# Optimization experiments

Measured on AMD Instinct MI355X. Metric: run time of the kernel, lower is better.

Reference implementation:

```python
import jax, jax.numpy as jnp
import numpy as np

B, N, D_IN, D_MEM = 32, 1024, 512, 512
LN_EPS = 1e-5


def setup_inputs() -> dict:
    key = jax.random.key(0)
    ks = jax.random.split(key, 6)
    adj = jax.random.uniform(ks[0], (B, N, N), dtype=jnp.float32)
    input_emb = jax.random.normal(ks[1], (B * N, D_IN), dtype=jnp.float32)
    seq_lens = jnp.full((B,), N, dtype=jnp.int64) if jax.config.jax_enable_x64 else jnp.full((B,), N, dtype=jnp.int32)
    scale = 1.0 / np.sqrt(D_IN)
    W0_w = jax.random.normal(ks[2], (D_MEM, D_IN), dtype=jnp.float32) * scale
    W0_b = jax.random.normal(ks[3], (D_MEM,), dtype=jnp.float32) * 0.01
    W1_w = jax.random.normal(ks[4], (D_MEM, D_MEM), dtype=jnp.float32) * scale
    W1_b = jax.random.normal(ks[5], (D_MEM,), dtype=jnp.float32) * 0.01
    ln_g = jnp.ones((D_MEM,), dtype=jnp.float32)
    ln_b = jnp.zeros((D_MEM,), dtype=jnp.float32)
    return {"adj": adj, "input_emb": input_emb, "seq_lens": seq_lens,
            "W0_w": W0_w, "W0_b": W0_b, "W1_w": W1_w, "W1_b": W1_b,
            "ln_g": ln_g, "ln_b": ln_b}


def _layer_norm(x, g, b):
    mu = jnp.mean(x, axis=-1, keepdims=True)
    var = jnp.mean(jnp.square(x - mu), axis=-1, keepdims=True)
    return (x - mu) * jax.lax.rsqrt(var + LN_EPS) * g + b


def reference(adj, input_emb, seq_lens, W0_w, W0_b, W1_w, W1_b, ln_g, ln_b):
    # All seq_lens == N, so pad_sequence(split(input_emb)) is a pure reshape.
    x = input_emb.reshape(B, N, D_IN)  # dropout probs are 0 -> identity
    denom = jnp.sum(adj, axis=2, keepdims=True) + 1.0           # [B,N,1]
    masks = ((jnp.sum(adj, axis=2) + jnp.sum(adj, axis=1)) == 0)[..., None]  # [B,N,1]
    for Ww, Wb in ((W0_w, W0_b), (W1_w, W1_b)):
        Ax = jnp.einsum('bnm,bmd->bnd', adj, x)                 # adj.bmm(x)
        # W(Ax) + W(x) == (Ax + x) @ W^T + 2b
        AxW = (Ax + x) @ Ww.T + 2.0 * Wb
        x = jax.nn.relu(AxW / denom)                            # gcn_drop p=0
    out = _layer_norm(x, ln_g, ln_b)                            # norm_flag=True
    return out, masks
```

## Files before the change

### kernel.cpp

```cpp
#include <hip/hip_runtime.h>
#include <stdint.h>

typedef __bf16 bf16_t;
typedef __bf16 bf16x8 __attribute__((ext_vector_type(8)));
typedef float  f32x4  __attribute__((ext_vector_type(4)));

#define GLD_LDS(gp, lp) __builtin_amdgcn_global_load_lds( \
    (const __attribute__((address_space(1))) void*)(gp),  \
    (__attribute__((address_space(3))) void*)(lp), 16, 0, 0)

__global__ void probe_kernel(const unsigned int* __restrict__ w, int* __restrict__ flag)
{
    const int lane = threadIdx.x;
    bool ok = true;
#pragma unroll
    for (int i = 0; i < 4; ++i) {
        unsigned x = w[lane * 4 + i];
        unsigned lo = x & 0xffffu, hi = x >> 16;
        ok = ok && (lo <= 0x3F80u) && (hi <= 0x3F80u);
    }
    unsigned long long m = __ballot(ok);
    if (lane == 0) *flag = (m == ~0ULL) ? 1 : 0;
}

#define STAGE_HALF(dstE, gp) do { \
    GLD_LDS((gp) + (size_t)r0 * K + cS,        lds + (dstE) + t * 8); \
    GLD_LDS((gp) + (size_t)(r0 + 64) * K + cS, lds + (dstE) + 4096 + t * 8); } while (0)

#define STG_A(d, h, k0) STAGE_HALF((d)*16384 + (h)*8192, Ag + (size_t)(h)*128*K + (k0))
#define STG_B(d, h, k0) STAGE_HALF(32768 + (d)*16384 + (h)*8192, Bg + (size_t)(h)*128*K + (k0))

#define LDA(af, d, mq) do { _Pragma("unroll") for (int i_ = 0; i_ < 4; ++i_) { \
    const bf16_t* p_ = lds + (d)*16384 + aBase + (((mq)*64) + (i_ << 4) + lrow) * 64; \
    af[i_][0] = *(const bf16x8*)(p_ + so0); \
    af[i_][1] = *(const bf16x8*)(p_ + so1); } } while (0)

#define LDB(bfv, d, nq) do { _Pragma("unroll") for (int j_ = 0; j_ < 2; ++j_) { \
    const bf16_t* p_ = lds + bBase + (d)*16384 + (((nq)*32) + (j_ << 4) + lrow) * 64; \
    bfv[j_][0] = *(const bf16x8*)(p_ + so0); \
    bfv[j_][1] = *(const bf16x8*)(p_ + so1); } } while (0)

#define MFMA_Q(af, bfv, mq, nq) do { _Pragma("unroll") for (int i_ = 0; i_ < 4; ++i_) \
    _Pragma("unroll") for (int j_ = 0; j_ < 2; ++j_) { \
    acc[(mq)*4+i_][(nq)*2+j_] = __builtin_amdgcn_mfma_f32_16x16x32_bf16(af[i_][0], bfv[j_][0], acc[(mq)*4+i_][(nq)*2+j_], 0, 0, 0); \
    acc[(mq)*4+i_][(nq)*2+j_] = __builtin_amdgcn_mfma_f32_16x16x32_bf16(af[i_][1], bfv[j_][1], acc[(mq)*4+i_][(nq)*2+j_], 0, 0, 0); } } while (0)

#define PHASE_SYNC() do { __builtin_amdgcn_s_barrier(); \
    asm volatile("s_waitcnt lgkmcnt(0)" ::: "memory"); \
    __builtin_amdgcn_sched_barrier(0); \
    __builtin_amdgcn_s_setprio(1); } while (0)

#define PHASE_END() do { __builtin_amdgcn_s_setprio(0); \
    __builtin_amdgcn_s_barrier(); } while (0)

#define PHASE_END_VM() do { __builtin_amdgcn_s_setprio(0); \
    asm volatile("s_waitcnt vmcnt(4)" ::: "memory"); \
    __builtin_amdgcn_s_barrier(); } while (0)

__device__ __forceinline__ void gemm256_mainloop(const bf16_t* __restrict__ Ag,
                                                 const bf16_t* __restrict__ Bg,
                                                 const int K, bf16_t* lds,
                                                 f32x4 acc[8][4])
{
    const int t    = threadIdx.x;
    const int wave = t >> 6;
    const int lane = t & 63;
    const int wr   = wave >> 2;
    const int wc   = wave & 3;
    const int lrow = lane & 15;
    const int quad = lane >> 4;
    const int g    = lrow & 7;

    const int r0 = t >> 3;
    const int cS = ((t & 7) ^ ((t >> 3) & 7)) << 3;

    const int aBase = wr * 8192;
    const int bBase = 32768 + ((wc >> 1) * 8192) + ((wc & 1) * 4096);
    const int so0 = (quad ^ g) << 3;
    const int so1 = ((4 | quad) ^ g) << 3;

#pragma unroll
    for (int i = 0; i < 8; ++i)
#pragma unroll
        for (int j = 0; j < 4; ++j)
#pragma unroll
            for (int r = 0; r < 4; ++r) acc[i][j][r] = 0.0f;

    STG_A(0, 0, 0); STG_A(0, 1, 0);
    STG_B(0, 0, 0); STG_B(0, 1, 0);
    STG_B(1, 0, 64); STG_B(1, 1, 64);
    asm volatile("s_waitcnt vmcnt(4)" ::: "memory");
    __builtin_amdgcn_s_barrier();

    const int NT  = K >> 6;
    const int NIT = NT >> 1;

    bf16x8 af0[4][2], af1[4][2], ba[2][2], bb[2][2];

    for (int it = 0; it < NIT; ++it) {
        const int kA1 = (2 * it + 1) << 6;
        const int k2  = ((2 * it + 2) < NT ? (2 * it + 2) : 0) << 6;
        const int k3  = ((2 * it + 3) < NT ? (2 * it + 3) : 0) << 6;

        LDA(af0, 0, 0); LDB(ba, 0, 0); STG_A(1, 0, kA1);
        PHASE_SYNC(); MFMA_Q(af0, ba, 0, 0); PHASE_END();

        LDB(bb, 0, 1); STG_A(1, 1, kA1);
        PHASE_SYNC(); MFMA_Q(af0, bb, 0, 1); PHASE_END();

        LDA(af1, 0, 1); STG_B(0, 0, k2);
        PHASE_SYNC(); MFMA_Q(af1, ba, 1, 0); PHASE_END();

        STG_B(0, 1, k2);
        PHASE_SYNC(); MFMA_Q(af1, bb, 1, 1); PHASE_END_VM();

        LDA(af0, 1, 0); LDB(ba, 1, 0); STG_A(0, 0, k2);
        PHASE_SYNC(); MFMA_Q(af0, ba, 0, 0); PHASE_END();

        LDB(bb, 1, 1); STG_A(0, 1, k2);
        PHASE_SYNC(); MFMA_Q(af0, bb, 0, 1); PHASE_END();

        LDA(af1, 1, 1); STG_B(1, 0, k3);
        PHASE_SYNC(); MFMA_Q(af1, ba, 1, 0); PHASE_END();

        STG_B(1, 1, k3);
        PHASE_SYNC(); MFMA_Q(af1, bb, 1, 1); PHASE_END_VM();
    }
    asm volatile("s_waitcnt vmcnt(0)" ::: "memory");
}

__global__ __launch_bounds__(512, 2) void bmm_kernel(const void* __restrict__ adj_in,
                                                     const bf16_t* __restrict__ adj_ws,
                                                     const bf16_t* __restrict__ xT,
                                                     const void* __restrict__ xadd,
                                                     int xadd_bf16,
                                                     const int* __restrict__ flag,
                                                     bf16_t* __restrict__ zout)
{
    extern __shared__ __align__(16) bf16_t lds[];
    const int is_bf = *flag;
    const bf16_t* adj = is_bf ? (const bf16_t*)adj_in : adj_ws;
    const int id   = blockIdx.x;
    const int xcd  = id & 7;
    const int s    = id >> 3;
    const int b    = (xcd << 2) | (s >> 3);
    const int tl   = s & 7;
    const int mt   = tl >> 1;
    const int nt2  = tl & 1;
    const bf16_t* Ag = adj + (size_t)b * 1048576 + (size_t)mt * 262144;
    const bf16_t* Bg = xT  + (size_t)b * 524288  + (size_t)nt2 * 262144;
    f32x4 acc[8][4];
    gemm256_mainloop(Ag, Bg, 1024, lds, acc);

    const int lane = threadIdx.x & 63;
    const int wave = threadIdx.x >> 6;
    const int wr = wave >> 2, wc = wave & 3;
    const int lrow = lane & 15, quad = lane >> 4;
    const int xf32 = (!xadd_bf16) && (!is_bf);
    const size_t rowbase = (size_t)b * 1024 + mt * 256 + wr * 128;
    const int colbase = nt2 * 256 + wc * 64;
#pragma unroll
    for (int i = 0; i < 8; ++i)
#pragma unroll
        for (int j = 0; j < 4; ++j)
#pragma unroll
            for (int r = 0; r < 4; ++r) {
                size_t row = rowbase + (i << 4) + (quad << 2) + r;
                int col = colbase + (j << 4) + lrow;
                size_t idx = row * 512 + col;
                float xa = xf32 ? ((const float*)xadd)[idx]
                                : (float)((const bf16_t*)xadd)[idx];
                zout[idx] = (bf16_t)(acc[i][j][r] + xa);
            }
}

__global__ __launch_bounds__(512, 2) void wgemm_kernel(const bf16_t* __restrict__ z,
                                                       const bf16_t* __restrict__ W,
                                                       const float* __restrict__ bias,
                                                       const float* __restrict__ rowsum,
                                                       bf16_t* __restrict__ out)
{
    extern __shared__ __align__(16) bf16_t lds[];
    const int id  = blockIdx.x;
    const int xcd = id & 7;
    const int s   = id >> 3;
    const int mt  = (xcd << 4) | (s >> 1);
    const int nt2 = s & 1;
    const bf16_t* Ag = z + (size_t)mt * 131072;
    const bf16_t* Bg = W + (size_t)nt2 * 131072;
    f32x4 acc[8][4];
    gemm256_mainloop(Ag, Bg, 512, lds, acc);

    const int lane = threadIdx.x & 63;
    const int wave = threadIdx.x >> 6;
    const int wr = wave >> 2, wc = wave & 3;
    const int lrow = lane & 15, quad = lane >> 4;
    const int m0 = mt * 256 + wr * 128;
    const int n0 = nt2 * 256 + wc * 64;
    float bi[4];
#pragma unroll
    for (int j = 0; j < 4; ++j) bi[j] = 2.0f * bias[n0 + (j << 4) + lrow];
#pragma unroll
    for (int i = 0; i < 8; ++i)
#pragma unroll
        for (int r = 0; r < 4; ++r) {
            int row = m0 + (i << 4) + (quad << 2) + r;
            float inv_dn = 1.0f / (rowsum[row] + 1.0f);
#pragma unroll
            for (int j = 0; j < 4; ++j) {
                int col = n0 + (j << 4) + lrow;
                float v = fmaxf((acc[i][j][r] + bi[j]) * inv_dn, 0.0f);
                out[(size_t)row * 512 + col] = (bf16_t)v;
            }
        }
}

__global__ __launch_bounds__(256) void transpose_kernel(const void* __restrict__ in,
                                                        bf16_t* __restrict__ out,
                                                        const int* __restrict__ flag,
                                                        int force_bf16)
{
    __shared__ float tile[64][65];
    const int f32 = (!force_bf16) && (*flag == 0);
    const int b  = blockIdx.z;
    const int n0 = blockIdx.x * 64;
    const int d0 = blockIdx.y * 64;
    const int t  = threadIdx.x;
    const size_t base = ((size_t)b * 1024 + n0) * 512 + d0;
#pragma unroll
    for (int pass = 0; pass < 2; ++pass) {
        int r = pass * 32 + (t >> 3);
        int c = (t & 7) << 3;
        size_t off = base + (size_t)r * 512 + c;
        if (f32) {
            const float4* p = (const float4*)((const float*)in + off);
            float4 a = p[0], q = p[1];
            tile[r][c+0]=a.x; tile[r][c+1]=a.y; tile[r][c+2]=a.z; tile[r][c+3]=a.w;
            tile[r][c+4]=q.x; tile[r][c+5]=q.y; tile[r][c+6]=q.z; tile[r][c+7]=q.w;
        } else {
            bf16x8 v = *(const bf16x8*)((const bf16_t*)in + off);
#pragma unroll
            for (int k = 0; k < 8; ++k) tile[r][c + k] = (float)v[k];
        }
    }
    __syncthreads();
    bf16_t* dst = out + ((size_t)b * 512 + d0) * 1024 + n0;
#pragma unroll
    for (int pass = 0; pass < 2; ++pass) {
        int d = pass * 32 + (t >> 3);
        int c = (t & 7) << 3;
        bf16x8 v;
#pragma unroll
        for (int k = 0; k < 8; ++k) v[k] = (bf16_t)tile[c + k][d];
        *(bf16x8*)(dst + (size_t)d * 1024 + c) = v;
    }
}

__global__ __launch_bounds__(256) void adjrow_kernel(const void* __restrict__ adj,
                                                     const int* __restrict__ flag,
                                                     bf16_t* __restrict__ adj_b,
                                                     float* __restrict__ rowsum)
{
    const int row  = blockIdx.x * 4 + (threadIdx.x >> 6);
    const int lane = threadIdx.x & 63;
    const int f32  = (*flag == 0);
    const size_t base = (size_t)row * 1024 + lane * 16;
    float v[16];
    if (f32) {
        const float4* p = (const float4*)((const float*)adj + base);
#pragma unroll
        for (int i = 0; i < 4; ++i) {
            float4 q = p[i];
            v[i*4+0]=q.x; v[i*4+1]=q.y; v[i*4+2]=q.z; v[i*4+3]=q.w;
        }
    } else {
        const bf16x8* p = (const bf16x8*)((const bf16_t*)adj + base);
        bf16x8 q0 = p[0], q1 = p[1];
#pragma unroll
        for (int k = 0; k < 8; ++k) { v[k] = (float)q0[k]; v[8+k] = (float)q1[k]; }
    }
    float s = 0.0f;
#pragma unroll
    for (int k = 0; k < 16; ++k) s += v[k];
    if (f32) {
        bf16x8 o0, o1;
#pragma unroll
        for (int k = 0; k < 8; ++k) { o0[k] = (bf16_t)v[k]; o1[k] = (bf16_t)v[8+k]; }
        *(bf16x8*)(adj_b + base)     = o0;
        *(bf16x8*)(adj_b + base + 8) = o1;
    }
#pragma unroll
    for (int off = 32; off > 0; off >>= 1) s += __shfl_down(s, off);
    if (lane == 0) rowsum[row] = s;
}

__global__ __launch_bounds__(256) void colsum_kernel(const void* __restrict__ adj_in,
                                                     const bf16_t* __restrict__ adj_ws,
                                                     const int* __restrict__ flag,
                                                     float* __restrict__ colsum)
{
    const bf16_t* a = (*flag) ? (const bf16_t*)adj_in : adj_ws;
    const int b = blockIdx.y;
    const int c = blockIdx.x * 256 + threadIdx.x;
    const int r0 = blockIdx.z * 256;
    const bf16_t* p = a + (size_t)b * 1048576 + (size_t)r0 * 1024 + c;
    float s = 0.0f;
#pragma unroll 8
    for (int r = 0; r < 256; ++r) s += (float)p[(size_t)r * 1024];
    atomicAdd(&colsum[b * 1024 + c], s);
}

__global__ __launch_bounds__(256) void mask_kernel(const float* __restrict__ rowsum,
                                                   const float* __restrict__ colsum,
                                                   void* __restrict__ out,
                                                   const int* __restrict__ flag)
{
    const int i = blockIdx.x * 256 + threadIdx.x;
    float m = (rowsum[i] + colsum[i] == 0.0f) ? 1.0f : 0.0f;
    if (*flag) ((bf16_t*)out)[16777216 + i] = (bf16_t)m;
    else       ((float*)out)[16777216 + i]  = m;
}

__global__ __launch_bounds__(256) void canon_small(const void* __restrict__ W0,
                                                   const void* __restrict__ W1,
                                                   const void* __restrict__ b0,
                                                   const void* __restrict__ b1,
                                                   const void* __restrict__ g,
                                                   const void* __restrict__ bt,
                                                   const int* __restrict__ flag,
                                                   bf16_t* __restrict__ W0ws,
                                                   bf16_t* __restrict__ W1ws,
                                                   float* __restrict__ par,
                                                   float* __restrict__ colsum)
{
    const int idx = blockIdx.x * 256 + threadIdx.x;
    const int f32 = (*flag == 0);
#define RD(p, i) (f32 ? ((const float*)(p))[i] : (float)((const bf16_t*)(p))[i])
    if      (idx < 262144) W0ws[idx]          = (bf16_t)RD(W0, idx);
    else if (idx < 524288) W1ws[idx - 262144] = (bf16_t)RD(W1, idx - 262144);
    else if (idx < 524800) par[idx - 524288]  = RD(b0, idx - 524288);
    else if (idx < 525312) par[idx - 524288]  = RD(b1, idx - 524800);
    else if (idx < 525824) par[idx - 524288]  = RD(g,  idx - 525312);
    else if (idx < 526336) par[idx - 524288]  = RD(bt, idx - 525824);
    else if (idx < 559104) colsum[idx - 526336] = 0.0f;
#undef RD
}

__global__ __launch_bounds__(256) void ln_kernel(const bf16_t* __restrict__ x,
                                                 const float* __restrict__ g,
                                                 const float* __restrict__ bb,
                                                 void* __restrict__ out,
                                                 const int* __restrict__ flag)
{
    const int row  = blockIdx.x * 4 + (threadIdx.x >> 6);
    const int lane = threadIdx.x & 63;
    bf16x8 xv = *(const bf16x8*)(x + (size_t)row * 512 + lane * 8);
    float vv[8], s = 0.0f, ss = 0.0f;
#pragma unroll
    for (int k = 0; k < 8; ++k) { vv[k] = (float)xv[k]; s += vv[k]; ss += vv[k] * vv[k]; }
#pragma unroll
    for (int off = 32; off > 0; off >>= 1) { s += __shfl_down(s, off); ss += __shfl_down(ss, off); }
    s = __shfl(s, 0); ss = __shfl(ss, 0);
    const float mu   = s * (1.0f / 512.0f);
    const float var  = ss * (1.0f / 512.0f) - mu * mu;
    const float rstd = rsqrtf(var + 1e-5f);
    float o[8];
#pragma unroll
    for (int k = 0; k < 8; ++k)
        o[k] = (vv[k] - mu) * rstd * g[lane * 8 + k] + bb[lane * 8 + k];
    const size_t obase = (size_t)row * 512 + lane * 8;
    if (*flag) {
        bf16x8 ob;
#pragma unroll
        for (int k = 0; k < 8; ++k) ob[k] = (bf16_t)o[k];
        *(bf16x8*)((bf16_t*)out + obase) = ob;
    } else {
        float4 o0 = {o[0], o[1], o[2], o[3]}, o1 = {o[4], o[5], o[6], o[7]};
        *(float4*)((float*)out + obase)     = o0;
        *(float4*)((float*)out + obase + 4) = o1;
    }
}

extern "C" void kernel_launch(void* const* d_in, const int* in_sizes, int n_in,
                              void* d_out, int out_size, void* d_ws, size_t ws_size,
                              hipStream_t stream)
{
    const void* adj  = d_in[0];
    const void* x0   = d_in[1];
    const void* W0w  = d_in[3];
    const void* W0b  = d_in[4];
    const void* W1w  = d_in[5];
    const void* W1b  = d_in[6];
    const void* lng  = d_in[7];
    const void* lnb  = d_in[8];

    char* ws = (char*)d_ws;
    bf16_t* adj_ws = (bf16_t*)ws;
    bf16_t* x2     = (bf16_t*)ws;
    bf16_t* z_buf  = (bf16_t*)(ws + 67108864);
    bf16_t* x1     = (bf16_t*)(ws + 100663296);
    bf16_t* W0ws   = (bf16_t*)(ws + 134217728);
    bf16_t* W1ws   = (bf16_t*)(ws + 134742016);
    float*  par    = (float*)(ws + 135266304);
    float*  rowsum = (float*)(ws + 135274496);
    float*  colsum = (float*)(ws + 135405568);
    int*    flag   = (int*)(ws + 135536640);

    bf16_t* xT = (bf16_t*)d_out;

    hipFuncSetAttribute((const void*)bmm_kernel,
                        hipFuncAttributeMaxDynamicSharedMemorySize, 131072);
    hipFuncSetAttribute((const void*)wgemm_kernel,
                        hipFuncAttributeMaxDynamicSharedMemorySize, 131072);

    probe_kernel<<<1, 64, 0, stream>>>((const unsigned int*)adj, flag);
    canon_small<<<2184, 256, 0, stream>>>(W0w, W1w, W0b, W1b, lng, lnb, flag,
                                          W0ws, W1ws, par, colsum);
    adjrow_kernel<<<8192, 256, 0, stream>>>(adj, flag, adj_ws, rowsum);
    colsum_kernel<<<dim3(4, 32, 4), 256, 0, stream>>>(adj, adj_ws, flag, colsum);
    mask_kernel<<<128, 256, 0, stream>>>(rowsum, colsum, d_out, flag);

    transpose_kernel<<<dim3(16, 8, 32), 256, 0, stream>>>(x0, xT, flag, 0);
    bmm_kernel<<<256, 512, 131072, stream>>>(adj, adj_ws, xT, x0, 0, flag, z_buf);
    wgemm_kernel<<<256, 512, 131072, stream>>>(z_buf, W0ws, par, rowsum, x1);

    transpose_kernel<<<dim3(16, 8, 32), 256, 0, stream>>>(x1, xT, flag, 1);
    bmm_kernel<<<256, 512, 131072, stream>>>(adj, adj_ws, xT, x1, 1, flag, z_buf);
    wgemm_kernel<<<256, 512, 131072, stream>>>(z_buf, W1ws, par + 512, rowsum, x2);

    ln_kernel<<<8192, 256, 0, stream>>>(x2, par + 1024, par + 1536, d_out, flag);
}
```

Measured before the change: 492.9 us.

## Fuse colsum into adjrow pass and emit transposed activations from wgemm epilogue

The row-sum and column-sum passes over adj become one kernel: each block walks 64 rows, keeps per-column partial sums in registers, and does four atomic adds per thread, so adj is read once instead of twice. The first-layer wgemm epilogue also writes the transposed bf16 activations directly, which removes the separate transpose kernel between layers. The risks are per-row shuffle reductions plus poorly coalesced 8-byte transposed stores from the GEMM epilogue.

```diff
diff --git a/kernel.cpp b/kernel.cpp
--- a/kernel.cpp
+++ b/kernel.cpp
@@ -2,6 +2,7 @@
 #include <stdint.h>
 
 typedef __bf16 bf16_t;
+typedef __bf16 bf16x4 __attribute__((ext_vector_type(4)));
 typedef __bf16 bf16x8 __attribute__((ext_vector_type(8)));
 typedef float  f32x4  __attribute__((ext_vector_type(4)));
 
@@ -178,7 +179,8 @@
                                                        const bf16_t* __restrict__ W,
                                                        const float* __restrict__ bias,
                                                        const float* __restrict__ rowsum,
-                                                       bf16_t* __restrict__ out)
+                                                       bf16_t* __restrict__ out,
+                                                       bf16_t* __restrict__ xTout)
 {
     extern __shared__ __align__(16) bf16_t lds[];
     const int id  = blockIdx.x;
@@ -197,22 +199,30 @@
     const int lrow = lane & 15, quad = lane >> 4;
     const int m0 = mt * 256 + wr * 128;
     const int n0 = nt2 * 256 + wc * 64;
+    bf16_t* xtb = xTout ? (xTout + (size_t)(mt >> 2) * 524288) : (bf16_t*)0;
     float bi[4];
 #pragma unroll
     for (int j = 0; j < 4; ++j) bi[j] = 2.0f * bias[n0 + (j << 4) + lrow];
 #pragma unroll
-    for (int i = 0; i < 8; ++i)
-#pragma unroll
-        for (int r = 0; r < 4; ++r) {
-            int row = m0 + (i << 4) + (quad << 2) + r;
-            float inv_dn = 1.0f / (rowsum[row] + 1.0f);
-#pragma unroll
-            for (int j = 0; j < 4; ++j) {
-                int col = n0 + (j << 4) + lrow;
-                float v = fmaxf((acc[i][j][r] + bi[j]) * inv_dn, 0.0f);
-                out[(size_t)row * 512 + col] = (bf16_t)v;
+    for (int i = 0; i < 8; ++i) {
+        const int rowb = m0 + (i << 4) + (quad << 2);
+        float invd[4];
+#pragma unroll
+        for (int r = 0; r < 4; ++r) invd[r] = 1.0f / (rowsum[rowb + r] + 1.0f);
+#pragma unroll
+        for (int j = 0; j < 4; ++j) {
+            const int col = n0 + (j << 4) + lrow;
+            bf16x4 tv;
+#pragma unroll
+            for (int r = 0; r < 4; ++r) {
+                float v = fmaxf((acc[i][j][r] + bi[j]) * invd[r], 0.0f);
+                bf16_t bv = (bf16_t)v;
+                out[(size_t)(rowb + r) * 512 + col] = bv;
+                tv[r] = bv;
             }
+            if (xtb) *(bf16x4*)(xtb + (size_t)col * 1024 + (rowb & 1023)) = tv;
         }
+    }
 }
 
 __global__ __launch_bounds__(256) void transpose_kernel(const void* __restrict__ in,
@@ -259,55 +269,44 @@
 __global__ __launch_bounds__(256) void adjrow_kernel(const void* __restrict__ adj,
                                                      const int* __restrict__ flag,
                                                      bf16_t* __restrict__ adj_b,
-                                                     float* __restrict__ rowsum)
-{
-    const int row  = blockIdx.x * 4 + (threadIdx.x >> 6);
+                                                     float* __restrict__ rowsum,
+                                                     float* __restrict__ colsum)
+{
+    __shared__ float rpart[64][4];
+    const int f32  = (*flag == 0);
+    const int wave = threadIdx.x >> 6;
     const int lane = threadIdx.x & 63;
-    const int f32  = (*flag == 0);
-    const size_t base = (size_t)row * 1024 + lane * 16;
-    float v[16];
-    if (f32) {
-        const float4* p = (const float4*)((const float*)adj + base);
-#pragma unroll
-        for (int i = 0; i < 4; ++i) {
-            float4 q = p[i];
-            v[i*4+0]=q.x; v[i*4+1]=q.y; v[i*4+2]=q.z; v[i*4+3]=q.w;
+    const int r0   = blockIdx.x * 64;
+    const int c    = wave * 256 + lane * 4;
+    float ca0 = 0.0f, ca1 = 0.0f, ca2 = 0.0f, ca3 = 0.0f;
+    for (int r = 0; r < 64; ++r) {
+        const size_t base = (size_t)(r0 + r) * 1024 + c;
+        float v0, v1, v2, v3;
+        if (f32) {
+            float4 q = *(const float4*)((const float*)adj + base);
+            v0 = q.x; v1 = q.y; v2 = q.z; v3 = q.w;
+            bf16x4 o = { (bf16_t)v0, (bf16_t)v1, (bf16_t)v2, (bf16_t)v3 };
+            *(bf16x4*)(adj_b + base) = o;
+        } else {
+            bf16x4 q = *(const bf16x4*)((const bf16_t*)adj + base);
+            v0 = (float)q[0]; v1 = (float)q[1]; v2 = (float)q[2]; v3 = (float)q[3];
         }
-    } else {
-        const bf16x8* p = (const bf16x8*)((const bf16_t*)adj + base);
-        bf16x8 q0 = p[0], q1 = p[1];
-#pragma unroll
-        for (int k = 0; k < 8; ++k) { v[k] = (float)q0[k]; v[8+k] = (float)q1[k]; }
-    }
-    float s = 0.0f;
-#pragma unroll
-    for (int k = 0; k < 16; ++k) s += v[k];
-    if (f32) {
-        bf16x8 o0, o1;
-#pragma unroll
-        for (int k = 0; k < 8; ++k) { o0[k] = (bf16_t)v[k]; o1[k] = (bf16_t)v[8+k]; }
-        *(bf16x8*)(adj_b + base)     = o0;
-        *(bf16x8*)(adj_b + base + 8) = o1;
-    }
-#pragma unroll
-    for (int off = 32; off > 0; off >>= 1) s += __shfl_down(s, off);
-    if (lane == 0) rowsum[row] = s;
-}
-
-__global__ __launch_bounds__(256) void colsum_kernel(const void* __restrict__ adj_in,
-                                                     const bf16_t* __restrict__ adj_ws,
-                                                     const int* __restrict__ flag,
-                                                     float* __restrict__ colsum)
-{
-    const bf16_t* a = (*flag) ? (const bf16_t*)adj_in : adj_ws;
-    const int b = blockIdx.y;
-    const int c = blockIdx.x * 256 + threadIdx.x;
-    const int r0 = blockIdx.z * 256;
-    const bf16_t* p = a + (size_t)b * 1048576 + (size_t)r0 * 1024 + c;
-    float s = 0.0f;
-#pragma unroll 8
-    for (int r = 0; r < 256; ++r) s += (float)p[(size_t)r * 1024];
-    atomicAdd(&colsum[b * 1024 + c], s);
+        ca0 += v0; ca1 += v1; ca2 += v2; ca3 += v3;
+        float sr = (v0 + v1) + (v2 + v3);
+#pragma unroll
+        for (int off = 32; off > 0; off >>= 1) sr += __shfl_down(sr, off);
+        if (lane == 0) rpart[r][wave] = sr;
+    }
+    __syncthreads();
+    if (threadIdx.x < 64) {
+        const int r = threadIdx.x;
+        rowsum[r0 + r] = (rpart[r][0] + rpart[r][1]) + (rpart[r][2] + rpart[r][3]);
+    }
+    float* cb = colsum + (size_t)(r0 >> 10) * 1024 + c;
+    atomicAdd(cb + 0, ca0);
+    atomicAdd(cb + 1, ca1);
+    atomicAdd(cb + 2, ca2);
+    atomicAdd(cb + 3, ca3);
 }
 
 __global__ __launch_bounds__(256) void mask_kernel(const float* __restrict__ rowsum,
@@ -416,17 +415,16 @@
     probe_kernel<<<1, 64, 0, stream>>>((const unsigned int*)adj, flag);
     canon_small<<<2184, 256, 0, stream>>>(W0w, W1w, W0b, W1b, lng, lnb, flag,
                                           W0ws, W1ws, par, colsum);
-    adjrow_kernel<<<8192, 256, 0, stream>>>(adj, flag, adj_ws, rowsum);
-    colsum_kernel<<<dim3(4, 32, 4), 256, 0, stream>>>(adj, adj_ws, flag, colsum);
+    adjrow_kernel<<<512, 256, 0, stream>>>(adj, flag, adj_ws, rowsum, colsum);
     mask_kernel<<<128, 256, 0, stream>>>(rowsum, colsum, d_out, flag);
 
     transpose_kernel<<<dim3(16, 8, 32), 256, 0, stream>>>(x0, xT, flag, 0);
     bmm_kernel<<<256, 512, 131072, stream>>>(adj, adj_ws, xT, x0, 0, flag, z_buf);
-    wgemm_kernel<<<256, 512, 131072, stream>>>(z_buf, W0ws, par, rowsum, x1);
-
-    transpose_kernel<<<dim3(16, 8, 32), 256, 0, stream>>>(x1, xT, flag, 1);
+    wgemm_kernel<<<256, 512, 131072, stream>>>(z_buf, W0ws, par, rowsum, x1, xT);
+
     bmm_kernel<<<256, 512, 131072, stream>>>(adj, adj_ws, xT, x1, 1, flag, z_buf);
-    wgemm_kernel<<<256, 512, 131072, stream>>>(z_buf, W1ws, par + 512, rowsum, x2);
+    wgemm_kernel<<<256, 512, 131072, stream>>>(z_buf, W1ws, par + 512, rowsum, x2,
+                                               (bf16_t*)0);
 
     ln_kernel<<<8192, 256, 0, stream>>>(x2, par + 1024, par + 1536, d_out, flag);
 }
```

New measurement: 489.0 us. No clear change (-0.8%).
